# Performance work log

Measured on AMD Instinct MI355X. Metric: run time of the kernel, lower is better.

The kernel has to match this reference:

```python
import jax, jax.numpy as jnp
import numpy as np

IN_SIZE = 1024
OUT_SIZE = 1024
HEAD_NUM = 16
KEY_SIZE = OUT_SIZE // HEAD_NUM  # 64
MIN_VALUE = float(np.finfo(np.float32).min / 2.0)
LN_EPS = 1e-5


def setup_inputs() -> dict:
    key = jax.random.key(0)
    ks = jax.random.split(key, 12)
    B, L = 4, 1024
    s_in = 1.0 / np.sqrt(IN_SIZE)
    s_out = 1.0 / np.sqrt(OUT_SIZE)
    x = jax.random.normal(ks[0], (B, L, IN_SIZE), dtype=jnp.float32)
    mask = jax.random.randint(ks[1], (B, L), 0, 2, dtype=jnp.int32)
    # Per-head linears stacked: [H, in, key_size] (already transposed for x @ W)
    Wq = jax.random.normal(ks[2], (HEAD_NUM, IN_SIZE, KEY_SIZE), dtype=jnp.float32) * s_in
    bq = jax.random.normal(ks[3], (HEAD_NUM, KEY_SIZE), dtype=jnp.float32) * s_in
    Wk = jax.random.normal(ks[4], (HEAD_NUM, IN_SIZE, KEY_SIZE), dtype=jnp.float32) * s_in
    bk = jax.random.normal(ks[5], (HEAD_NUM, KEY_SIZE), dtype=jnp.float32) * s_in
    Wv = jax.random.normal(ks[6], (HEAD_NUM, IN_SIZE, KEY_SIZE), dtype=jnp.float32) * s_in
    bv = jax.random.normal(ks[7], (HEAD_NUM, KEY_SIZE), dtype=jnp.float32) * s_in
    Wo = jax.random.normal(ks[8], (OUT_SIZE, OUT_SIZE), dtype=jnp.float32) * s_out
    bo = jax.random.normal(ks[9], (OUT_SIZE,), dtype=jnp.float32) * s_out
    gamma = jnp.ones((OUT_SIZE,), dtype=jnp.float32)
    beta = jnp.zeros((OUT_SIZE,), dtype=jnp.float32)
    return {"x": x, "mask": mask, "Wq": Wq, "bq": bq, "Wk": Wk, "bk": bk,
            "Wv": Wv, "bv": bv, "Wo": Wo, "bo": bo, "gamma": gamma, "beta": beta}


def _attention(x, mask, Wq, bq, Wk, bk, Wv, bv, Wo, bo, gamma, beta):
    # Per-head projections, batched over heads: [B, H, L, d]
    q = jnp.einsum('bli,hid->bhld', x, Wq) + bq[None, :, None, :]
    k = jnp.einsum('bli,hid->bhld', x, Wk) + bk[None, :, None, :]
    v = jnp.einsum('bli,hid->bhld', x, Wv) + bv[None, :, None, :]
    scale = 1.0 / np.sqrt(KEY_SIZE)
    score = jnp.einsum('bhld,bhmd->bhlm', q, k) * scale  # [B, H, L, L]
    # masked_fill((mask == 0).unsqueeze(-2), min_value): mask over key positions
    score = jnp.where((mask == 0)[:, None, None, :], MIN_VALUE, score)
    atten = jax.nn.softmax(score, axis=-1)  # [B, H, L, L]
    value = jnp.einsum('bhlm,bhmd->bhld', atten, v)
    # concat heads -> [B, L, H*d] then output linear
    B, H, L, d = value.shape
    value = value.transpose(0, 2, 1, 3).reshape(B, L, H * d)
    value = value @ Wo.T + bo
    # wo_resize=False and in_size == out_size -> nearest interpolate is identity
    bypass = x
    pre = bypass + value
    mu = jnp.mean(pre, axis=-1, keepdims=True)
    var = jnp.mean(jnp.square(pre - mu), axis=-1, keepdims=True)
    out = (pre - mu) * jax.lax.rsqrt(var + LN_EPS) * gamma + beta
    return out, atten


def reference(x, mask, Wq, bq, Wk, bk, Wv, bv, Wo, bo, gamma, beta):
    return _attention(x, mask, Wq, bq, Wk, bk, Wv, bv, Wo, bo, gamma, beta)
```

## Files before the change

### kernel.cpp

```cpp
#include <hip/hip_runtime.h>
#include <hip/hip_bf16.h>

typedef __bf16 bf16x8 __attribute__((ext_vector_type(8)));
typedef __bf16 bf16x4 __attribute__((ext_vector_type(4)));
typedef float  f32x4  __attribute__((ext_vector_type(4)));

#define MIN_VALUE (-1.7014118346046923e38f)

__device__ __forceinline__ void async_load16(const __bf16* g, __bf16* l) {
    __builtin_amdgcn_global_load_lds(
        (const __attribute__((address_space(1))) uint32_t*)(uintptr_t)g,
        (__attribute__((address_space(3))) uint32_t*)(uint32_t)(uintptr_t)l,
        16, 0, 0);
}

__global__ __launch_bounds__(256) void conv_x_kernel(const float* __restrict__ x,
                                                     __bf16* __restrict__ xh) {
    int i = (blockIdx.x * 256 + threadIdx.x) * 4;
    float4 v = *(const float4*)(x + i);
    float vv[4] = {v.x, v.y, v.z, v.w};
    bf16x4 h;
    for (int e = 0; e < 4; ++e) h[e] = (__bf16)vv[e];
    *(bf16x4*)(xh + i) = h;
}

__global__ __launch_bounds__(256) void split_w_kernel(const float* __restrict__ Wq,
                                                      const float* __restrict__ Wk,
                                                      const float* __restrict__ Wv,
                                                      __bf16* __restrict__ wh,
                                                      __bf16* __restrict__ wl) {
    __shared__ float t[32][33];
    int z = blockIdx.z;
    int sel = z >> 4, h = z & 15;
    const float* W = (sel == 0) ? Wq : (sel == 1) ? Wk : Wv;
    int i0 = blockIdx.x * 32, d0 = blockIdx.y * 32;
    int tx = threadIdx.x & 31, ty = threadIdx.x >> 5;
    for (int it = 0; it < 4; ++it) {
        int r = ty + it * 8;
        t[r][tx] = W[(size_t)(h * 1024 + i0 + r) * 64 + d0 + tx];
    }
    __syncthreads();
    for (int it = 0; it < 4; ++it) {
        int r = ty + it * 8;
        float v = t[tx][r];
        size_t o = (size_t)(sel * 1024 + h * 64 + d0 + r) * 1024 + i0 + tx;
        __bf16 hi = (__bf16)v;
        wh[o] = hi;
        wl[o] = (__bf16)(v - (float)hi);
    }
}

__global__ __launch_bounds__(256) void conv_wo_kernel(const float* __restrict__ Wo,
                                                      __bf16* __restrict__ wob) {
    int i = (blockIdx.x * 256 + threadIdx.x) * 4;
    float4 v = *(const float4*)(Wo + i);
    float vv[4] = {v.x, v.y, v.z, v.w};
    bf16x4 h;
    for (int e = 0; e < 4; ++e) h[e] = (__bf16)vv[e];
    *(bf16x4*)(wob + i) = h;
}

__global__ __launch_bounds__(256) void qkv_gemm_kernel(
    const __bf16* __restrict__ xh,
    const __bf16* __restrict__ wh, const __bf16* __restrict__ wl,
    const float* __restrict__ bq, const float* __restrict__ bk, const float* __restrict__ bv,
    __bf16* __restrict__ qb, __bf16* __restrict__ kb, __bf16* __restrict__ vtb) {
    __shared__ __bf16 As[128 * 32];
    __shared__ __bf16 Bh[128 * 32];
    __shared__ __bf16 Bl[128 * 32];
    const int tid = threadIdx.x;
    const int m0 = blockIdx.y * 128;
    const int n0 = blockIdx.x * 128;
    const int lane = tid & 63, w = tid >> 6;
    const int l15 = lane & 15, quad = lane >> 4;
    const int wm = (w & 1) * 64, wn = (w >> 1) * 64;
    const int r4 = lane >> 2;
    const int c8 = (lane & 3) * 8;

    f32x4 acc[4][4];
    for (int i = 0; i < 4; ++i)
        for (int j = 0; j < 4; ++j)
            for (int r = 0; r < 4; ++r) acc[i][j][r] = 0.0f;

    for (int kk = 0; kk < 1024; kk += 32) {
        __syncthreads();
        for (int half = 0; half < 2; ++half) {
            int row = w * 32 + half * 16 + r4;
            int lo = w * 1024 + half * 512 + lane * 8;
            async_load16(&xh[(size_t)(m0 + row) * 1024 + kk + c8], &As[lo]);
            async_load16(&wh[(size_t)(n0 + row) * 1024 + kk + c8], &Bh[lo]);
            async_load16(&wl[(size_t)(n0 + row) * 1024 + kk + c8], &Bl[lo]);
        }
        __syncthreads();
        bf16x8 af[4], bhf[4], blf[4];
        for (int i = 0; i < 4; ++i)
            af[i] = *(const bf16x8*)&As[(wm + i * 16 + l15) * 32 + quad * 8];
        for (int j = 0; j < 4; ++j) {
            bhf[j] = *(const bf16x8*)&Bh[(wn + j * 16 + l15) * 32 + quad * 8];
            blf[j] = *(const bf16x8*)&Bl[(wn + j * 16 + l15) * 32 + quad * 8];
        }
        for (int i = 0; i < 4; ++i)
            for (int j = 0; j < 4; ++j) {
                acc[i][j] = __builtin_amdgcn_mfma_f32_16x16x32_bf16(af[i], bhf[j], acc[i][j], 0, 0, 0);
                acc[i][j] = __builtin_amdgcn_mfma_f32_16x16x32_bf16(af[i], blf[j], acc[i][j], 0, 0, 0);
            }
    }

    const int sel = n0 >> 10;
    const float* bias = (sel == 0) ? bq : (sel == 1) ? bk : bv;
    for (int i = 0; i < 4; ++i)
        for (int j = 0; j < 4; ++j)
            for (int r = 0; r < 4; ++r) {
                int m = m0 + wm + i * 16 + quad * 4 + r;
                int n = n0 + wn + j * 16 + l15;
                int nn = n & 1023;
                int h = nn >> 6, d = n & 63;
                float v = acc[i][j][r] + bias[nn];
                int bb = m >> 10, ll = m & 1023;
                if (sel == 2) {
                    vtb[(size_t)((bb * 16 + h) * 64 + d) * 1024 + ll] = (__bf16)v;
                } else {
                    __bf16* dst = (sel == 0) ? qb : kb;
                    dst[(size_t)((bb * 16 + h) * 1024 + ll) * 64 + d] = (__bf16)v;
                }
            }
}

__global__ __launch_bounds__(256) void attn_kernel(
    const __bf16* __restrict__ qb, const __bf16* __restrict__ kb,
    const __bf16* __restrict__ vtb, const int* __restrict__ mask,
    float* __restrict__ atten, __bf16* __restrict__ value_bf) {
    __shared__ float S[16 * 1024];
    const int m0 = blockIdx.x * 16;
    const int h = blockIdx.y, b = blockIdx.z;
    const int bh = b * 16 + h;
    const int tid = threadIdx.x;
    const int lane = tid & 63, w = tid >> 6;
    const int l15 = lane & 15, quad = lane >> 4;

    const __bf16* qbase = qb + (size_t)(bh * 1024 + m0 + l15) * 64 + quad * 8;
    bf16x8 a0 = *(const bf16x8*)(qbase);
    bf16x8 a1 = *(const bf16x8*)(qbase + 32);
    const int swz1 = quad << 4;
    for (int t = 0; t < 16; ++t) {
        int n0 = w * 256 + t * 16;
        const __bf16* kbase = kb + (size_t)(bh * 1024 + n0 + l15) * 64 + quad * 8;
        bf16x8 b0 = *(const bf16x8*)(kbase);
        bf16x8 b1 = *(const bf16x8*)(kbase + 32);
        f32x4 c = {0.f, 0.f, 0.f, 0.f};
        c = __builtin_amdgcn_mfma_f32_16x16x32_bf16(a0, b0, c, 0, 0, 0);
        c = __builtin_amdgcn_mfma_f32_16x16x32_bf16(a1, b1, c, 0, 0, 0);
        int col = n0 + l15;
        bool msk = (mask[b * 1024 + col] == 0);
        for (int r = 0; r < 4; ++r) {
            float s = c[r] * 0.125f;
            if (msk) s = MIN_VALUE;
            S[(quad * 4 + r) * 1024 + (col ^ swz1)] = s;
        }
    }
    __syncthreads();

    float p[4][16];
    const int swz2 = w << 4;
    for (int j = 0; j < 4; ++j) {
        int row = w * 4 + j;
        float mx = -3.4e38f;
        for (int i = 0; i < 16; ++i) {
            p[j][i] = S[row * 1024 + ((i * 64 + lane) ^ swz2)];
            mx = fmaxf(mx, p[j][i]);
        }
        for (int o = 32; o > 0; o >>= 1) mx = fmaxf(mx, __shfl_xor(mx, o));
        float sum = 0.f;
        for (int i = 0; i < 16; ++i) {
            float e = __expf(p[j][i] - mx);
            p[j][i] = e;
            sum += e;
        }
        for (int o = 32; o > 0; o >>= 1) sum += __shfl_xor(sum, o);
        float inv = 1.0f / sum;
        float* out = atten + (size_t)(bh * 1024 + m0 + row) * 1024;
        for (int i = 0; i < 16; ++i) {
            p[j][i] *= inv;
            out[i * 64 + lane] = p[j][i];
        }
    }
    __syncthreads();

    __bf16* Sb = (__bf16*)S;
    for (int j = 0; j < 4; ++j) {
        int row = w * 4 + j;
        for (int i = 0; i < 16; ++i) Sb[row * 1040 + i * 64 + lane] = (__bf16)p[j][i];
    }
    __syncthreads();

    f32x4 acc = {0.f, 0.f, 0.f, 0.f};
    const __bf16* vbase = vtb + (size_t)(bh * 64 + w * 16 + l15) * 1024 + quad * 8;
    for (int kk = 0; kk < 1024; kk += 32) {
        bf16x8 af = *(const bf16x8*)&Sb[l15 * 1040 + kk + quad * 8];
        bf16x8 bf_ = *(const bf16x8*)(vbase + kk);
        acc = __builtin_amdgcn_mfma_f32_16x16x32_bf16(af, bf_, acc, 0, 0, 0);
    }
    for (int r = 0; r < 4; ++r) {
        int mrow = quad * 4 + r;
        value_bf[(size_t)(b * 1024 + m0 + mrow) * 1024 + h * 64 + w * 16 + l15] = (__bf16)acc[r];
    }
}

__global__ __launch_bounds__(256) void outproj_kernel(
    const __bf16* __restrict__ vb, const __bf16* __restrict__ wob,
    const float* __restrict__ x, const float* __restrict__ bo,
    float* __restrict__ pre) {
    __shared__ __bf16 As[128 * 32];
    __shared__ __bf16 Bs[128 * 32];
    const int tid = threadIdx.x;
    const int m0 = blockIdx.y * 128;
    const int n0 = blockIdx.x * 128;
    const int lane = tid & 63, w = tid >> 6;
    const int l15 = lane & 15, quad = lane >> 4;
    const int wm = (w & 1) * 64, wn = (w >> 1) * 64;
    const int r4 = lane >> 2;
    const int c8 = (lane & 3) * 8;

    f32x4 acc[4][4];
    for (int i = 0; i < 4; ++i)
        for (int j = 0; j < 4; ++j)
            for (int r = 0; r < 4; ++r) acc[i][j][r] = 0.0f;

    for (int kk = 0; kk < 1024; kk += 32) {
        __syncthreads();
        for (int half = 0; half < 2; ++half) {
            int row = w * 32 + half * 16 + r4;
            int lo = w * 1024 + half * 512 + lane * 8;
            async_load16(&vb[(size_t)(m0 + row) * 1024 + kk + c8], &As[lo]);
            async_load16(&wob[(size_t)(n0 + row) * 1024 + kk + c8], &Bs[lo]);
        }
        __syncthreads();
        bf16x8 af[4], bfr[4];
        for (int i = 0; i < 4; ++i) af[i] = *(const bf16x8*)&As[(wm + i * 16 + l15) * 32 + quad * 8];
        for (int j = 0; j < 4; ++j) bfr[j] = *(const bf16x8*)&Bs[(wn + j * 16 + l15) * 32 + quad * 8];
        for (int i = 0; i < 4; ++i)
            for (int j = 0; j < 4; ++j)
                acc[i][j] = __builtin_amdgcn_mfma_f32_16x16x32_bf16(af[i], bfr[j], acc[i][j], 0, 0, 0);
    }

    for (int i = 0; i < 4; ++i)
        for (int j = 0; j < 4; ++j)
            for (int r = 0; r < 4; ++r) {
                int m = m0 + wm + i * 16 + quad * 4 + r;
                int n = n0 + wn + j * 16 + l15;
                pre[(size_t)m * 1024 + n] = acc[i][j][r] + x[(size_t)m * 1024 + n] + bo[n];
            }
}

__global__ __launch_bounds__(256) void ln_kernel(float* __restrict__ buf,
                                                 const float* __restrict__ gamma,
                                                 const float* __restrict__ beta) {
    const int row = blockIdx.x;
    const int tid = threadIdx.x;
    const int lane = tid & 63, w = tid >> 6;
    __shared__ float red[8];
    float* rp = buf + (size_t)row * 1024;
    float loc[4];
    float s = 0.f, s2 = 0.f;
    for (int e = 0; e < 4; ++e) {
        loc[e] = rp[tid + e * 256];
        s += loc[e];
        s2 += loc[e] * loc[e];
    }
    for (int o = 32; o > 0; o >>= 1) {
        s += __shfl_xor(s, o);
        s2 += __shfl_xor(s2, o);
    }
    if (lane == 0) { red[w * 2] = s; red[w * 2 + 1] = s2; }
    __syncthreads();
    float ts = red[0] + red[2] + red[4] + red[6];
    float ts2 = red[1] + red[3] + red[5] + red[7];
    float mu = ts * (1.0f / 1024.0f);
    float var = ts2 * (1.0f / 1024.0f) - mu * mu;
    float sc = rsqrtf(var + 1e-5f);
    for (int e = 0; e < 4; ++e) {
        int c = tid + e * 256;
        rp[c] = (loc[e] - mu) * sc * gamma[c] + beta[c];
    }
}

extern "C" void kernel_launch(void* const* d_in, const int* in_sizes, int n_in,
                              void* d_out, int out_size, void* d_ws, size_t ws_size,
                              hipStream_t stream) {
    const float* x    = (const float*)d_in[0];
    const int*   mask = (const int*)d_in[1];
    const float* Wq   = (const float*)d_in[2];
    const float* bq   = (const float*)d_in[3];
    const float* Wk   = (const float*)d_in[4];
    const float* bk   = (const float*)d_in[5];
    const float* Wv   = (const float*)d_in[6];
    const float* bv   = (const float*)d_in[7];
    const float* Wo   = (const float*)d_in[8];
    const float* bo   = (const float*)d_in[9];
    const float* gamma= (const float*)d_in[10];
    const float* beta = (const float*)d_in[11];

    char* p = (char*)d_ws;
    __bf16* xh    = (__bf16*)p; p += (size_t)4194304 * 2;
    __bf16* wt_hi = (__bf16*)p; p += (size_t)3145728 * 2;
    __bf16* wt_lo = (__bf16*)p; p += (size_t)3145728 * 2;
    __bf16* wob   = (__bf16*)p; p += (size_t)1048576 * 2;
    __bf16* qb    = (__bf16*)p; p += (size_t)4194304 * 2;
    __bf16* kb    = (__bf16*)p; p += (size_t)4194304 * 2;
    __bf16* vtb   = (__bf16*)p; p += (size_t)4194304 * 2;
    __bf16* valb  = (__bf16*)p; p += (size_t)4194304 * 2;

    float* outb  = (float*)d_out;
    float* atten = outb + 4194304;

    conv_x_kernel<<<4096, 256, 0, stream>>>(x, xh);
    split_w_kernel<<<dim3(32, 2, 48), 256, 0, stream>>>(Wq, Wk, Wv, wt_hi, wt_lo);
    conv_wo_kernel<<<1024, 256, 0, stream>>>(Wo, wob);
    qkv_gemm_kernel<<<dim3(24, 32), 256, 0, stream>>>(xh, wt_hi, wt_lo, bq, bk, bv, qb, kb, vtb);
    attn_kernel<<<dim3(64, 16, 4), 256, 0, stream>>>(qb, kb, vtb, mask, atten, valb);
    outproj_kernel<<<dim3(8, 32), 256, 0, stream>>>(valb, wob, x, bo, outb);
    ln_kernel<<<4096, 256, 0, stream>>>(outb, gamma, beta);
}
```

Measured before the change: 553.2 us.

## Keep attention scores in registers and skip low-weight split for V projection

The attention kernel now keeps the score tile in registers and reduces the row max and sum across waves through a small shared buffer. It stores unnormalized bf16 probabilities to LDS and applies the 1/sum to the PV output, which removes the fp32 score round-trip through LDS and two barriers. The smaller LDS footprint and launch bounds target more resident blocks. In the QKV GEMM, V-column tiles skip the low-part weight loads and MFMAs, trading some V precision for less work.

```diff
diff --git a/kernel.cpp b/kernel.cpp
--- a/kernel.cpp
+++ b/kernel.cpp
@@ -76,6 +76,7 @@
     const int wm = (w & 1) * 64, wn = (w >> 1) * 64;
     const int r4 = lane >> 2;
     const int c8 = (lane & 3) * 8;
+    const bool need_lo = (n0 < 2048);
 
     f32x4 acc[4][4];
     for (int i = 0; i < 4; ++i)
@@ -89,21 +90,25 @@
             int lo = w * 1024 + half * 512 + lane * 8;
             async_load16(&xh[(size_t)(m0 + row) * 1024 + kk + c8], &As[lo]);
             async_load16(&wh[(size_t)(n0 + row) * 1024 + kk + c8], &Bh[lo]);
-            async_load16(&wl[(size_t)(n0 + row) * 1024 + kk + c8], &Bl[lo]);
+            if (need_lo)
+                async_load16(&wl[(size_t)(n0 + row) * 1024 + kk + c8], &Bl[lo]);
         }
         __syncthreads();
         bf16x8 af[4], bhf[4], blf[4];
         for (int i = 0; i < 4; ++i)
             af[i] = *(const bf16x8*)&As[(wm + i * 16 + l15) * 32 + quad * 8];
-        for (int j = 0; j < 4; ++j) {
+        for (int j = 0; j < 4; ++j)
             bhf[j] = *(const bf16x8*)&Bh[(wn + j * 16 + l15) * 32 + quad * 8];
-            blf[j] = *(const bf16x8*)&Bl[(wn + j * 16 + l15) * 32 + quad * 8];
-        }
+        if (need_lo)
+            for (int j = 0; j < 4; ++j)
+                blf[j] = *(const bf16x8*)&Bl[(wn + j * 16 + l15) * 32 + quad * 8];
         for (int i = 0; i < 4; ++i)
-            for (int j = 0; j < 4; ++j) {
+            for (int j = 0; j < 4; ++j)
                 acc[i][j] = __builtin_amdgcn_mfma_f32_16x16x32_bf16(af[i], bhf[j], acc[i][j], 0, 0, 0);
-                acc[i][j] = __builtin_amdgcn_mfma_f32_16x16x32_bf16(af[i], blf[j], acc[i][j], 0, 0, 0);
-            }
+        if (need_lo)
+            for (int i = 0; i < 4; ++i)
+                for (int j = 0; j < 4; ++j)
+                    acc[i][j] = __builtin_amdgcn_mfma_f32_16x16x32_bf16(af[i], blf[j], acc[i][j], 0, 0, 0);
     }
 
     const int sel = n0 >> 10;
@@ -126,11 +131,12 @@
             }
 }
 
-__global__ __launch_bounds__(256) void attn_kernel(
+__global__ __launch_bounds__(256, 4) void attn_kernel(
     const __bf16* __restrict__ qb, const __bf16* __restrict__ kb,
     const __bf16* __restrict__ vtb, const int* __restrict__ mask,
     float* __restrict__ atten, __bf16* __restrict__ value_bf) {
-    __shared__ float S[16 * 1024];
+    __shared__ __bf16 P[16 * 1048];
+    __shared__ float red[2][4][16];
     const int m0 = blockIdx.x * 16;
     const int h = blockIdx.y, b = blockIdx.z;
     const int bh = b * 16 + h;
@@ -141,7 +147,7 @@
     const __bf16* qbase = qb + (size_t)(bh * 1024 + m0 + l15) * 64 + quad * 8;
     bf16x8 a0 = *(const bf16x8*)(qbase);
     bf16x8 a1 = *(const bf16x8*)(qbase + 32);
-    const int swz1 = quad << 4;
+    f32x4 s[16];
     for (int t = 0; t < 16; ++t) {
         int n0 = w * 256 + t * 16;
         const __bf16* kbase = kb + (size_t)(bh * 1024 + n0 + l15) * 64 + quad * 8;
@@ -150,59 +156,65 @@
         f32x4 c = {0.f, 0.f, 0.f, 0.f};
         c = __builtin_amdgcn_mfma_f32_16x16x32_bf16(a0, b0, c, 0, 0, 0);
         c = __builtin_amdgcn_mfma_f32_16x16x32_bf16(a1, b1, c, 0, 0, 0);
-        int col = n0 + l15;
-        bool msk = (mask[b * 1024 + col] == 0);
+        bool msk = (mask[b * 1024 + n0 + l15] == 0);
+        for (int r = 0; r < 4; ++r) s[t][r] = msk ? MIN_VALUE : c[r] * 0.125f;
+    }
+
+    float mx[4];
+    for (int r = 0; r < 4; ++r) {
+        float m = s[0][r];
+        for (int t = 1; t < 16; ++t) m = fmaxf(m, s[t][r]);
+        for (int o = 1; o < 16; o <<= 1) m = fmaxf(m, __shfl_xor(m, o));
+        mx[r] = m;
+    }
+    if (l15 == 0)
+        for (int r = 0; r < 4; ++r) red[0][w][quad * 4 + r] = mx[r];
+    __syncthreads();
+    for (int r = 0; r < 4; ++r) {
+        int row = quad * 4 + r;
+        mx[r] = fmaxf(fmaxf(red[0][0][row], red[0][1][row]),
+                      fmaxf(red[0][2][row], red[0][3][row]));
+    }
+
+    float sum[4] = {0.f, 0.f, 0.f, 0.f};
+    for (int t = 0; t < 16; ++t)
         for (int r = 0; r < 4; ++r) {
-            float s = c[r] * 0.125f;
-            if (msk) s = MIN_VALUE;
-            S[(quad * 4 + r) * 1024 + (col ^ swz1)] = s;
+            float e = __expf(s[t][r] - mx[r]);
+            s[t][r] = e;
+            sum[r] += e;
+            P[(quad * 4 + r) * 1048 + w * 256 + t * 16 + l15] = (__bf16)e;
         }
-    }
+    for (int r = 0; r < 4; ++r) {
+        float sm = sum[r];
+        for (int o = 1; o < 16; o <<= 1) sm += __shfl_xor(sm, o);
+        sum[r] = sm;
+    }
+    if (l15 == 0)
+        for (int r = 0; r < 4; ++r) red[1][w][quad * 4 + r] = sum[r];
     __syncthreads();
-
-    float p[4][16];
-    const int swz2 = w << 4;
-    for (int j = 0; j < 4; ++j) {
-        int row = w * 4 + j;
-        float mx = -3.4e38f;
-        for (int i = 0; i < 16; ++i) {
-            p[j][i] = S[row * 1024 + ((i * 64 + lane) ^ swz2)];
-            mx = fmaxf(mx, p[j][i]);
-        }
-        for (int o = 32; o > 0; o >>= 1) mx = fmaxf(mx, __shfl_xor(mx, o));
-        float sum = 0.f;
-        for (int i = 0; i < 16; ++i) {
-            float e = __expf(p[j][i] - mx);
-            p[j][i] = e;
-            sum += e;
-        }
-        for (int o = 32; o > 0; o >>= 1) sum += __shfl_xor(sum, o);
-        float inv = 1.0f / sum;
-        float* out = atten + (size_t)(bh * 1024 + m0 + row) * 1024;
-        for (int i = 0; i < 16; ++i) {
-            p[j][i] *= inv;
-            out[i * 64 + lane] = p[j][i];
-        }
-    }
-    __syncthreads();
-
-    __bf16* Sb = (__bf16*)S;
-    for (int j = 0; j < 4; ++j) {
-        int row = w * 4 + j;
-        for (int i = 0; i < 16; ++i) Sb[row * 1040 + i * 64 + lane] = (__bf16)p[j][i];
-    }
-    __syncthreads();
+    float inv[4];
+    for (int r = 0; r < 4; ++r) {
+        int row = quad * 4 + r;
+        inv[r] = 1.0f / (red[1][0][row] + red[1][1][row] +
+                         red[1][2][row] + red[1][3][row]);
+    }
+
+    for (int r = 0; r < 4; ++r) {
+        float* out = atten + (size_t)(bh * 1024 + m0 + quad * 4 + r) * 1024 + w * 256 + l15;
+        for (int t = 0; t < 16; ++t) out[t * 16] = s[t][r] * inv[r];
+    }
 
     f32x4 acc = {0.f, 0.f, 0.f, 0.f};
     const __bf16* vbase = vtb + (size_t)(bh * 64 + w * 16 + l15) * 1024 + quad * 8;
     for (int kk = 0; kk < 1024; kk += 32) {
-        bf16x8 af = *(const bf16x8*)&Sb[l15 * 1040 + kk + quad * 8];
+        bf16x8 af = *(const bf16x8*)&P[l15 * 1048 + kk + quad * 8];
         bf16x8 bf_ = *(const bf16x8*)(vbase + kk);
         acc = __builtin_amdgcn_mfma_f32_16x16x32_bf16(af, bf_, acc, 0, 0, 0);
     }
     for (int r = 0; r < 4; ++r) {
         int mrow = quad * 4 + r;
-        value_bf[(size_t)(b * 1024 + m0 + mrow) * 1024 + h * 64 + w * 16 + l15] = (__bf16)acc[r];
+        value_bf[(size_t)(b * 1024 + m0 + mrow) * 1024 + h * 64 + w * 16 + l15] =
+            (__bf16)(acc[r] * inv[r]);
     }
 }
 
```

Result: faster. 522.2 us (-5.6%).
